# Kernel tuning notes

Hardware: AMD Instinct MI355X
Metric: run time of the kernel (lower is better)

The kernel has to match this reference:

```python
import jax, jax.numpy as jnp
import numpy as np

HEADS = 4
HID = 256
MAX_OFFSET = 2


def setup_inputs() -> dict:
    key = jax.random.key(0)
    ks = jax.random.split(key, 8)
    B, T, C = 4, 512, HID
    x = jax.random.normal(ks[0], (B, T, C), jnp.float32)
    mask = jax.random.randint(ks[1], (B, 1, T), 0, 2).astype(bool)
    s2 = 1.0 / np.sqrt(2 * C)
    s1 = 1.0 / np.sqrt(C)
    W_subj = jax.random.uniform(ks[2], (2 * C, C), jnp.float32, -s2, s2)
    b_subj = jax.random.uniform(ks[3], (C,), jnp.float32, -s2, s2)
    W_obj = jax.random.uniform(ks[4], (2 * C, C), jnp.float32, -s2, s2)
    b_obj = jax.random.uniform(ks[5], (C,), jnp.float32, -s2, s2)
    W_t = jax.random.uniform(ks[6], (C, HEADS), jnp.float32, -s1, s1)
    b_t = jax.random.uniform(ks[7], (HEADS,), jnp.float32, -s1, s1)
    return {"x": x, "W_subj": W_subj, "b_subj": b_subj, "W_obj": W_obj,
            "b_obj": b_obj, "W_t": W_t, "b_t": b_t, "mask": mask}


def reference(x, W_subj, b_subj, W_obj, b_obj, W_t, b_t, mask):
    # x: [B,T,C]. torch MaxPool1d on [B,T,C] pools over the LAST dim (C),
    # kernel = 2*MAX_OFFSET+1, stride 1, same padding (pad value -inf).
    k = 2 * MAX_OFFSET + 1
    x_pooled = jax.lax.reduce_window(
        x, -jnp.inf, jax.lax.max,
        window_dimensions=(1, 1, k), window_strides=(1, 1, 1),
        padding=[(0, 0), (0, 0), (MAX_OFFSET, MAX_OFFSET)])
    x_new = jnp.concatenate([x_pooled, x], axis=2)      # [B,T,2C]
    subj = x_new @ W_subj + b_subj                      # [B,T,C]
    obj = x_new @ W_obj + b_obj                         # [B,T,C]
    # subj.unsqueeze(1): varies over axis 2; obj.unsqueeze(2): varies over axis 1
    abs_multi = jnp.abs(subj[:, None, :, :] - obj[:, :, None, :])  # [B,T,T,C]
    rep = abs_multi @ W_t + b_t                         # [B,T,T,H]
    attn = jax.nn.softmax(jax.nn.relu(rep), axis=2)     # softmax over obj axis
    m = mask[:, 0, :]                                   # [B,T]
    mm = m[:, None, :] & m[:, :, None]                  # [B,T,T]
    attn = jnp.where(mm[..., None], 0.0, attn)          # masked_fill -> 0
    return x_new, attn  # attn[..., h] == attn_adj_list[h]
```

## Files before the change

### kernel.cpp

```cpp
#include <hip/hip_runtime.h>
#include <hip/hip_bf16.h>
#include <math.h>

#define NB 4
#define NT 512
#define NC 256
#define NC2 512
#define NH 4

typedef __attribute__((ext_vector_type(8))) short bf16x8;
typedef __attribute__((ext_vector_type(4))) float f32x4;
typedef __attribute__((ext_vector_type(2))) float f32x2;

__device__ inline unsigned short f2bf(float f) {
    unsigned u = __float_as_uint(f);
    unsigned r = (u + 0x7fffu + ((u >> 16) & 1u)) >> 16;
    return (unsigned short)r;
}

__global__ void k_mask(const unsigned char* __restrict__ raw, int* __restrict__ out) {
    __shared__ int s_bytes;
    if (threadIdx.x == 0) s_bytes = 0;
    __syncthreads();
    int flag = 0;
    const unsigned* w = (const unsigned*)raw;
    for (int i = threadIdx.x; i < (NB * NT) / 4; i += blockDim.x)
        if (w[i] > 1u) flag = 1;
    if (flag) atomicOr(&s_bytes, 1);
    __syncthreads();
    const int ib = s_bytes;
    for (int i = threadIdx.x; i < NB * NT; i += blockDim.x) {
        int v = ib ? (int)raw[i] : ((const int*)raw)[i];
        out[i] = v ? 1 : 0;
    }
}

__global__ void k_pool(const float* __restrict__ x, float* __restrict__ xnew,
                       unsigned short* __restrict__ xb) {
    const int row = blockIdx.x;
    const int c = threadIdx.x;
    __shared__ float r[NC];
    r[c] = x[(size_t)row * NC + c];
    __syncthreads();
    float m = r[c];
    if (c >= 1) m = fmaxf(m, r[c - 1]);
    if (c >= 2) m = fmaxf(m, r[c - 2]);
    if (c <= 254) m = fmaxf(m, r[c + 1]);
    if (c <= 253) m = fmaxf(m, r[c + 2]);
    float* o = xnew + (size_t)row * NC2;
    o[c] = m;
    o[NC + c] = r[c];
    unsigned short* ob = xb + (size_t)row * NC2;
    ob[c] = f2bf(m);
    ob[NC + c] = f2bf(r[c]);
}

__global__ void k_wcast(const float* __restrict__ Ws, const float* __restrict__ Wo,
                        unsigned short* __restrict__ wbt) {
    __shared__ float lds[32][33];
    const int kb = blockIdx.x >> 4;
    const int nb = blockIdx.x & 15;
    const int tx = threadIdx.x & 31;
    const int ty8 = threadIdx.x >> 5;
    const int n0 = nb * 32;
    const int k0 = kb * 32;
    const float* src = (n0 < 256) ? Ws : Wo;
    const int ncol = n0 & 255;
#pragma unroll
    for (int rr = 0; rr < 4; ++rr) {
        int kl = ty8 * 4 + rr;
        lds[kl][tx] = src[(size_t)(k0 + kl) * NC + ncol + tx];
    }
    __syncthreads();
#pragma unroll
    for (int rr = 0; rr < 4; ++rr) {
        int nl = ty8 * 4 + rr;
        wbt[(size_t)(n0 + nl) * NC2 + k0 + tx] = f2bf(lds[tx][nl]);
    }
}

#define MFMA_B16(A, B, C) __builtin_amdgcn_mfma_f32_16x16x32_bf16(A, B, C, 0, 0, 0)
__global__ __launch_bounds__(256) void k_gemm(
    const unsigned short* __restrict__ xb, const unsigned short* __restrict__ wbt,
    const float* __restrict__ bs, const float* __restrict__ bo,
    float* __restrict__ subj, float* __restrict__ obj) {
    const int bx = blockIdx.x;
    const int m0 = (bx >> 3) * 64;
    const int n0 = (bx & 7) * 64;
    const int w = threadIdx.x >> 6, lane = threadIdx.x & 63;
    const int wm = m0 + (w >> 1) * 32;
    const int wn = n0 + (w & 1) * 32;
    const int r = lane & 15, kg = lane >> 4;

    const unsigned short* aB0 = xb + (size_t)(wm + r) * NC2 + kg * 8;
    const unsigned short* aB1 = aB0 + 16 * NC2;
    const unsigned short* bB0 = wbt + (size_t)(wn + r) * NC2 + kg * 8;
    const unsigned short* bB1 = bB0 + 16 * NC2;

    f32x4 acc00 = {0.f, 0.f, 0.f, 0.f}, acc01 = {0.f, 0.f, 0.f, 0.f};
    f32x4 acc10 = {0.f, 0.f, 0.f, 0.f}, acc11 = {0.f, 0.f, 0.f, 0.f};

    bf16x8 a0 = *(const bf16x8*)(aB0);
    bf16x8 a1 = *(const bf16x8*)(aB1);
    bf16x8 b0 = *(const bf16x8*)(bB0);
    bf16x8 b1 = *(const bf16x8*)(bB1);

    for (int kk = 0; kk < NC2; kk += 64) {
        bf16x8 a0n = *(const bf16x8*)(aB0 + kk + 32);
        bf16x8 a1n = *(const bf16x8*)(aB1 + kk + 32);
        bf16x8 b0n = *(const bf16x8*)(bB0 + kk + 32);
        bf16x8 b1n = *(const bf16x8*)(bB1 + kk + 32);
        acc00 = MFMA_B16(a0, b0, acc00);
        acc01 = MFMA_B16(a0, b1, acc01);
        acc10 = MFMA_B16(a1, b0, acc10);
        acc11 = MFMA_B16(a1, b1, acc11);
        if (kk + 64 < NC2) {
            a0 = *(const bf16x8*)(aB0 + kk + 64);
            a1 = *(const bf16x8*)(aB1 + kk + 64);
            b0 = *(const bf16x8*)(bB0 + kk + 64);
            b1 = *(const bf16x8*)(bB1 + kk + 64);
        }
        acc00 = MFMA_B16(a0n, b0n, acc00);
        acc01 = MFMA_B16(a0n, b1n, acc01);
        acc10 = MFMA_B16(a1n, b0n, acc10);
        acc11 = MFMA_B16(a1n, b1n, acc11);
    }

#define EPI(ACC, S, T) { \
    const int col = wn + (T) * 16 + r; \
    const int rowb = wm + (S) * 16 + kg * 4; \
    const float bias = (col < NC) ? bs[col] : bo[col - NC]; \
    float* outp = (col < NC) ? (subj + col) : (obj + col - NC); \
    _Pragma("unroll") \
    for (int e = 0; e < 4; ++e) outp[(size_t)(rowb + e) * NC] = ACC[e] + bias; }
    EPI(acc00, 0, 0) EPI(acc01, 0, 1) EPI(acc10, 1, 0) EPI(acc11, 1, 1)
#undef EPI
}

#define OF32(r) ((r) * 36 + (((r) >> 2) << 2))
__global__ __launch_bounds__(256, 3) void k_rep(
    const float* __restrict__ subj, const float* __restrict__ obj,
    const float* __restrict__ Wt, const float* __restrict__ bt,
    float* __restrict__ attn) {
    const int bx = blockIdx.x;
    const int b = bx >> 8;
    const int rem = bx & 255;
    const int it = rem >> 4, jt = rem & 15;
    const int i0 = it * 32, j0 = jt * 32;
    const int bNT = b * NT;

    __shared__ float lds_buf[4736];
    float* sjT = lds_buf;
    float* obT = lds_buf + 2368;

    const int tid = threadIdx.x;
    const int cs = __builtin_amdgcn_readfirstlane(tid >> 6);
    const int lane = tid & 63;
    const int tx4 = (lane & 7) * 4;
    const int ty4 = (lane >> 3) * 4;
    const int csB = cs * 16;

    const int c4a = tid & 15;
    const int jb = tid >> 4;

    const float4* WtV = (const float4*)Wt;

    f32x2 acc[4][2][4];
#pragma unroll
    for (int ii = 0; ii < 4; ++ii)
#pragma unroll
        for (int jp = 0; jp < 2; ++jp)
#pragma unroll
            for (int h = 0; h < 4; ++h) acc[ii][jp][h] = (f32x2){0.f, 0.f};

    float4 vs0, vs1, vo0, vo1;
#define LOADCH(CC) { \
    vs0 = *(const float4*)(subj + ((size_t)(bNT + j0 + jb)) * NC + (CC) + c4a * 4); \
    vs1 = *(const float4*)(subj + ((size_t)(bNT + j0 + jb + 16)) * NC + (CC) + c4a * 4); \
    vo0 = *(const float4*)(obj  + ((size_t)(bNT + i0 + jb)) * NC + (CC) + c4a * 4); \
    vo1 = *(const float4*)(obj  + ((size_t)(bNT + i0 + jb + 16)) * NC + (CC) + c4a * 4); }

    LOADCH(0)

    for (int cc = 0; cc < 4; ++cc) {
        const int cc64 = cc * 64;
        if (cc) __syncthreads();
        {
            const int rb = c4a * 4;
            sjT[OF32(rb + 0) + jb] = vs0.x; sjT[OF32(rb + 1) + jb] = vs0.y;
            sjT[OF32(rb + 2) + jb] = vs0.z; sjT[OF32(rb + 3) + jb] = vs0.w;
            sjT[OF32(rb + 0) + jb + 16] = vs1.x; sjT[OF32(rb + 1) + jb + 16] = vs1.y;
            sjT[OF32(rb + 2) + jb + 16] = vs1.z; sjT[OF32(rb + 3) + jb + 16] = vs1.w;
            obT[OF32(rb + 0) + jb] = vo0.x; obT[OF32(rb + 1) + jb] = vo0.y;
            obT[OF32(rb + 2) + jb] = vo0.z; obT[OF32(rb + 3) + jb] = vo0.w;
            obT[OF32(rb + 0) + jb + 16] = vo1.x; obT[OF32(rb + 1) + jb + 16] = vo1.y;
            obT[OF32(rb + 2) + jb + 16] = vo1.z; obT[OF32(rb + 3) + jb + 16] = vo1.w;
        }
        __syncthreads();
        if (cc + 1 < 4) LOADCH(cc64 + 64)

#pragma unroll 8
        for (int q = 0; q < 16; ++q) {
            const int cl = csB + q;
            const float4 sv4 = *(const float4*)&sjT[OF32(cl) + tx4];
            const float4 ov4 = *(const float4*)&obT[OF32(cl) + ty4];
            const float4 w4 = WtV[cc64 + cl];
            const f32x2 s01 = {sv4.x, sv4.y};
            const f32x2 s23 = {sv4.z, sv4.w};
            const f32x2 w0 = {w4.x, w4.x};
            const f32x2 w1 = {w4.y, w4.y};
            const f32x2 w2 = {w4.z, w4.z};
            const f32x2 w3 = {w4.w, w4.w};
#define IIBLK(II, OV) { \
    const f32x2 ob2 = {OV, OV}; \
    const f32x2 d01 = s01 - ob2; \
    const f32x2 d23 = s23 - ob2; \
    f32x2 a01, a23; \
    a01.x = fabsf(d01.x); a01.y = fabsf(d01.y); \
    a23.x = fabsf(d23.x); a23.y = fabsf(d23.y); \
    acc[II][0][0] = a01 * w0 + acc[II][0][0]; \
    acc[II][0][1] = a01 * w1 + acc[II][0][1]; \
    acc[II][0][2] = a01 * w2 + acc[II][0][2]; \
    acc[II][0][3] = a01 * w3 + acc[II][0][3]; \
    acc[II][1][0] = a23 * w0 + acc[II][1][0]; \
    acc[II][1][1] = a23 * w1 + acc[II][1][1]; \
    acc[II][1][2] = a23 * w2 + acc[II][1][2]; \
    acc[II][1][3] = a23 * w3 + acc[II][1][3]; }
            IIBLK(0, ov4.x) IIBLK(1, ov4.y) IIBLK(2, ov4.z) IIBLK(3, ov4.w)
#undef IIBLK
        }
    }
#undef LOADCH

    float* rbuf = lds_buf;
    const int lb = lane * 36;
#pragma unroll
    for (int half = 0; half < 2; ++half) {
        __syncthreads();
        if (cs == 1 || cs == 3) {
            float* p = rbuf + ((cs == 1) ? 0 : 2368) + lb;
#pragma unroll
            for (int k = 0; k < 16; ++k)
                *(f32x2*)(p + k * 2) = acc[half * 2 + (k >> 3)][(k >> 2) & 1][k & 3];
        }
        __syncthreads();
        if (cs == 0 || cs == 2) {
            const float* p = rbuf + ((cs == 0) ? 0 : 2368) + lb;
#pragma unroll
            for (int k = 0; k < 16; ++k)
                acc[half * 2 + (k >> 3)][(k >> 2) & 1][k & 3] += *(const f32x2*)(p + k * 2);
        }
    }
#pragma unroll
    for (int half = 0; half < 2; ++half) {
        __syncthreads();
        if (cs == 2) {
            float* p = rbuf + lb;
#pragma unroll
            for (int k = 0; k < 16; ++k)
                *(f32x2*)(p + k * 2) = acc[half * 2 + (k >> 3)][(k >> 2) & 1][k & 3];
        }
        __syncthreads();
        if (cs == 0) {
            const float* p = rbuf + lb;
#pragma unroll
            for (int k = 0; k < 16; ++k)
                acc[half * 2 + (k >> 3)][(k >> 2) & 1][k & 3] += *(const f32x2*)(p + k * 2);
        }
    }

    if (cs == 0) {
        const float4 btv = *(const float4*)bt;
#pragma unroll
        for (int ii = 0; ii < 4; ++ii) {
            const int i = i0 + ty4 + ii;
            float* orow = attn + (((size_t)(bNT + i)) * NT + (j0 + tx4)) * NH;
            float4 r0, r1, r2, r3;
            r0.x = fmaxf(acc[ii][0][0].x + btv.x, 0.f);
            r0.y = fmaxf(acc[ii][0][1].x + btv.y, 0.f);
            r0.z = fmaxf(acc[ii][0][2].x + btv.z, 0.f);
            r0.w = fmaxf(acc[ii][0][3].x + btv.w, 0.f);
            r1.x = fmaxf(acc[ii][0][0].y + btv.x, 0.f);
            r1.y = fmaxf(acc[ii][0][1].y + btv.y, 0.f);
            r1.z = fmaxf(acc[ii][0][2].y + btv.z, 0.f);
            r1.w = fmaxf(acc[ii][0][3].y + btv.w, 0.f);
            r2.x = fmaxf(acc[ii][1][0].x + btv.x, 0.f);
            r2.y = fmaxf(acc[ii][1][1].x + btv.y, 0.f);
            r2.z = fmaxf(acc[ii][1][2].x + btv.z, 0.f);
            r2.w = fmaxf(acc[ii][1][3].x + btv.w, 0.f);
            r3.x = fmaxf(acc[ii][1][0].y + btv.x, 0.f);
            r3.y = fmaxf(acc[ii][1][1].y + btv.y, 0.f);
            r3.z = fmaxf(acc[ii][1][2].y + btv.z, 0.f);
            r3.w = fmaxf(acc[ii][1][3].y + btv.w, 0.f);
            *(float4*)(orow + 0)  = r0;
            *(float4*)(orow + 4)  = r1;
            *(float4*)(orow + 8)  = r2;
            *(float4*)(orow + 12) = r3;
        }
    }
}

__global__ __launch_bounds__(256) void k_soft(float* __restrict__ attn,
                                              const int* __restrict__ mask) {
    const int wv = threadIdx.x >> 6, lane = threadIdx.x & 63;
    const int bi = blockIdx.x * 4 + wv;
    const int b = bi >> 9;
    float4* row = (float4*)(attn + (size_t)bi * (NT * NH));

    float4 v[8];
#pragma unroll
    for (int q = 0; q < 8; ++q) v[q] = row[lane + 64 * q];

    float mx[4];
#pragma unroll
    for (int h = 0; h < 4; ++h) {
        float m = ((const float*)&v[0])[h];
#pragma unroll
        for (int q = 1; q < 8; ++q) m = fmaxf(m, ((const float*)&v[q])[h]);
        mx[h] = m;
    }
#pragma unroll
    for (int off = 32; off; off >>= 1) {
#pragma unroll
        for (int h = 0; h < 4; ++h) mx[h] = fmaxf(mx[h], __shfl_xor(mx[h], off));
    }

    float sm[4] = {0.f, 0.f, 0.f, 0.f};
#pragma unroll
    for (int q = 0; q < 8; ++q) {
        float4 e;
        e.x = expf(v[q].x - mx[0]); e.y = expf(v[q].y - mx[1]);
        e.z = expf(v[q].z - mx[2]); e.w = expf(v[q].w - mx[3]);
        v[q] = e;
        sm[0] += e.x; sm[1] += e.y; sm[2] += e.z; sm[3] += e.w;
    }
#pragma unroll
    for (int off = 32; off; off >>= 1) {
#pragma unroll
        for (int h = 0; h < 4; ++h) sm[h] += __shfl_xor(sm[h], off);
    }
    float rinv[4];
#pragma unroll
    for (int h = 0; h < 4; ++h) rinv[h] = 1.0f / sm[h];

    const int mi = mask[bi];
#pragma unroll
    for (int q = 0; q < 8; ++q) {
        const int mj = mask[b * NT + lane + 64 * q];
        const bool z = (mi & mj);
        float4 o;
        o.x = z ? 0.f : v[q].x * rinv[0];
        o.y = z ? 0.f : v[q].y * rinv[1];
        o.z = z ? 0.f : v[q].z * rinv[2];
        o.w = z ? 0.f : v[q].w * rinv[3];
        row[lane + 64 * q] = o;
    }
}

extern "C" void kernel_launch(void* const* d_in, const int* in_sizes, int n_in,
                              void* d_out, int out_size, void* d_ws, size_t ws_size,
                              hipStream_t stream) {
    const float* x      = (const float*)d_in[0];
    const float* W_subj = (const float*)d_in[1];
    const float* b_subj = (const float*)d_in[2];
    const float* W_obj  = (const float*)d_in[3];
    const float* b_obj  = (const float*)d_in[4];
    const float* W_t    = (const float*)d_in[5];
    const float* b_t    = (const float*)d_in[6];
    const unsigned char* mask_raw = (const unsigned char*)d_in[7];

    float* xnew = (float*)d_out;
    float* attn = xnew + (size_t)NB * NT * NC2;

    int* wmask          = (int*)d_ws;
    float* subj         = (float*)((char*)d_ws + 8192);
    float* obj          = subj + (size_t)NB * NT * NC;
    unsigned short* xb  = (unsigned short*)(obj + (size_t)NB * NT * NC);
    unsigned short* wbt = xb + (size_t)NB * NT * NC2;

    hipLaunchKernelGGL(k_mask, dim3(1), dim3(256), 0, stream, mask_raw, wmask);
    hipLaunchKernelGGL(k_pool, dim3(NB * NT), dim3(NC), 0, stream, x, xnew, xb);
    hipLaunchKernelGGL(k_wcast, dim3(256), dim3(256), 0, stream, W_subj, W_obj, wbt);
    hipLaunchKernelGGL(k_gemm, dim3(256), dim3(256), 0, stream,
                       xb, wbt, b_subj, b_obj, subj, obj);
    hipLaunchKernelGGL(k_rep, dim3(NB * 16 * 16), dim3(256), 0, stream,
                       subj, obj, W_t, b_t, attn);
    hipLaunchKernelGGL(k_soft, dim3(NB * NT / 4), dim3(256), 0, stream, attn, wmask);
}
```

Measured before the change: 137.2 us.

## Rewrite |s-o| as 2*max(s,o)-s-o and fuse prep kernels

The inner rep loop now uses |s-o| = 2*max(s,o) - s - o. This replaces sub+abs with a single max per element, while the linear s·Wt and o·Wt terms are precomputed per row by a new small k_sw kernel and added in the epilogue. The mask, pool and weight-cast kernels are merged into one prep launch to cut launch overhead. The trade-off is one extra kernel launch and slightly different rounding, since the result is now formed as a difference of larger values.

```diff
diff --git a/kernel.cpp b/kernel.cpp
--- a/kernel.cpp
+++ b/kernel.cpp
@@ -18,28 +18,17 @@
     return (unsigned short)r;
 }
 
-__global__ void k_mask(const unsigned char* __restrict__ raw, int* __restrict__ out) {
-    __shared__ int s_bytes;
-    if (threadIdx.x == 0) s_bytes = 0;
-    __syncthreads();
-    int flag = 0;
-    const unsigned* w = (const unsigned*)raw;
-    for (int i = threadIdx.x; i < (NB * NT) / 4; i += blockDim.x)
-        if (w[i] > 1u) flag = 1;
-    if (flag) atomicOr(&s_bytes, 1);
-    __syncthreads();
-    const int ib = s_bytes;
-    for (int i = threadIdx.x; i < NB * NT; i += blockDim.x) {
-        int v = ib ? (int)raw[i] : ((const int*)raw)[i];
-        out[i] = v ? 1 : 0;
-    }
-}
-
-__global__ void k_pool(const float* __restrict__ x, float* __restrict__ xnew,
-                       unsigned short* __restrict__ xb) {
+__global__ __launch_bounds__(256) void k_prep(
+    const float* __restrict__ x, const unsigned char* __restrict__ raw,
+    const float* __restrict__ Ws, const float* __restrict__ Wo,
+    float* __restrict__ xnew, unsigned short* __restrict__ xb,
+    int* __restrict__ wmask, unsigned short* __restrict__ wbt) {
     const int row = blockIdx.x;
     const int c = threadIdx.x;
     __shared__ float r[NC];
+    __shared__ float wl[32][33];
+    __shared__ int s_bytes;
+
     r[c] = x[(size_t)row * NC + c];
     __syncthreads();
     float m = r[c];
@@ -53,29 +42,41 @@
     unsigned short* ob = xb + (size_t)row * NC2;
     ob[c] = f2bf(m);
     ob[NC + c] = f2bf(r[c]);
-}
-
-__global__ void k_wcast(const float* __restrict__ Ws, const float* __restrict__ Wo,
-                        unsigned short* __restrict__ wbt) {
-    __shared__ float lds[32][33];
-    const int kb = blockIdx.x >> 4;
-    const int nb = blockIdx.x & 15;
-    const int tx = threadIdx.x & 31;
-    const int ty8 = threadIdx.x >> 5;
-    const int n0 = nb * 32;
-    const int k0 = kb * 32;
-    const float* src = (n0 < 256) ? Ws : Wo;
-    const int ncol = n0 & 255;
-#pragma unroll
-    for (int rr = 0; rr < 4; ++rr) {
-        int kl = ty8 * 4 + rr;
-        lds[kl][tx] = src[(size_t)(k0 + kl) * NC + ncol + tx];
-    }
-    __syncthreads();
-#pragma unroll
-    for (int rr = 0; rr < 4; ++rr) {
-        int nl = ty8 * 4 + rr;
-        wbt[(size_t)(n0 + nl) * NC2 + k0 + tx] = f2bf(lds[tx][nl]);
+
+    if (row == 0) {
+        if (c == 0) s_bytes = 0;
+        __syncthreads();
+        int flag = 0;
+        const unsigned* w = (const unsigned*)raw;
+        for (int i = c; i < (NB * NT) / 4; i += 256)
+            if (w[i] > 1u) flag = 1;
+        if (flag) atomicOr(&s_bytes, 1);
+        __syncthreads();
+        const int ib = s_bytes;
+        for (int i = c; i < NB * NT; i += 256) {
+            int v = ib ? (int)raw[i] : ((const int*)raw)[i];
+            wmask[i] = v ? 1 : 0;
+        }
+    }
+
+    if (row >= 1 && row <= 256) {
+        const int t = row - 1;
+        const int kb = t >> 4, nb = t & 15;
+        const int tx = c & 31, ty8 = c >> 5;
+        const int n0 = nb * 32, k0 = kb * 32;
+        const float* src = (n0 < 256) ? Ws : Wo;
+        const int ncol = n0 & 255;
+#pragma unroll
+        for (int rr = 0; rr < 4; ++rr) {
+            int kl = ty8 * 4 + rr;
+            wl[kl][tx] = src[(size_t)(k0 + kl) * NC + ncol + tx];
+        }
+        __syncthreads();
+#pragma unroll
+        for (int rr = 0; rr < 4; ++rr) {
+            int nl = ty8 * 4 + rr;
+            wbt[(size_t)(n0 + nl) * NC2 + k0 + tx] = f2bf(wl[tx][nl]);
+        }
     }
 }
 
@@ -137,10 +138,37 @@
 #undef EPI
 }
 
+__global__ __launch_bounds__(256) void k_sw(
+    const float* __restrict__ subj, const float* __restrict__ obj,
+    const float* __restrict__ Wt, float* __restrict__ Sw, float* __restrict__ Ow) {
+    const int gw = blockIdx.x * 4 + (threadIdx.x >> 6);
+    const int lane = threadIdx.x & 63;
+    const int mat = gw & 1;
+    const int row = gw >> 1;
+    const float* src = mat ? obj : subj;
+    const float4 xv = *(const float4*)(src + (size_t)row * NC + lane * 4);
+    const float4* WtV = (const float4*)Wt;
+    float4 a = {0.f, 0.f, 0.f, 0.f};
+#pragma unroll
+    for (int e = 0; e < 4; ++e) {
+        const float4 wv = WtV[lane * 4 + e];
+        const float xe = (e == 0) ? xv.x : (e == 1) ? xv.y : (e == 2) ? xv.z : xv.w;
+        a.x = fmaf(xe, wv.x, a.x); a.y = fmaf(xe, wv.y, a.y);
+        a.z = fmaf(xe, wv.z, a.z); a.w = fmaf(xe, wv.w, a.w);
+    }
+#pragma unroll
+    for (int off = 32; off; off >>= 1) {
+        a.x += __shfl_xor(a.x, off); a.y += __shfl_xor(a.y, off);
+        a.z += __shfl_xor(a.z, off); a.w += __shfl_xor(a.w, off);
+    }
+    if (lane == 0) ((float4*)(mat ? Ow : Sw))[row] = a;
+}
+
 #define OF32(r) ((r) * 36 + (((r) >> 2) << 2))
 __global__ __launch_bounds__(256, 3) void k_rep(
     const float* __restrict__ subj, const float* __restrict__ obj,
     const float* __restrict__ Wt, const float* __restrict__ bt,
+    const float* __restrict__ Sw, const float* __restrict__ Ow,
     float* __restrict__ attn) {
     const int bx = blockIdx.x;
     const int b = bx >> 8;
@@ -213,19 +241,16 @@
             const f32x2 w3 = {w4.w, w4.w};
 #define IIBLK(II, OV) { \
     const f32x2 ob2 = {OV, OV}; \
-    const f32x2 d01 = s01 - ob2; \
-    const f32x2 d23 = s23 - ob2; \
-    f32x2 a01, a23; \
-    a01.x = fabsf(d01.x); a01.y = fabsf(d01.y); \
-    a23.x = fabsf(d23.x); a23.y = fabsf(d23.y); \
-    acc[II][0][0] = a01 * w0 + acc[II][0][0]; \
-    acc[II][0][1] = a01 * w1 + acc[II][0][1]; \
-    acc[II][0][2] = a01 * w2 + acc[II][0][2]; \
-    acc[II][0][3] = a01 * w3 + acc[II][0][3]; \
-    acc[II][1][0] = a23 * w0 + acc[II][1][0]; \
-    acc[II][1][1] = a23 * w1 + acc[II][1][1]; \
-    acc[II][1][2] = a23 * w2 + acc[II][1][2]; \
-    acc[II][1][3] = a23 * w3 + acc[II][1][3]; }
+    const f32x2 m01 = __builtin_elementwise_max(s01, ob2); \
+    const f32x2 m23 = __builtin_elementwise_max(s23, ob2); \
+    acc[II][0][0] = __builtin_elementwise_fma(m01, w0, acc[II][0][0]); \
+    acc[II][0][1] = __builtin_elementwise_fma(m01, w1, acc[II][0][1]); \
+    acc[II][0][2] = __builtin_elementwise_fma(m01, w2, acc[II][0][2]); \
+    acc[II][0][3] = __builtin_elementwise_fma(m01, w3, acc[II][0][3]); \
+    acc[II][1][0] = __builtin_elementwise_fma(m23, w0, acc[II][1][0]); \
+    acc[II][1][1] = __builtin_elementwise_fma(m23, w1, acc[II][1][1]); \
+    acc[II][1][2] = __builtin_elementwise_fma(m23, w2, acc[II][1][2]); \
+    acc[II][1][3] = __builtin_elementwise_fma(m23, w3, acc[II][1][3]); }
             IIBLK(0, ov4.x) IIBLK(1, ov4.y) IIBLK(2, ov4.z) IIBLK(3, ov4.w)
 #undef IIBLK
         }
@@ -271,27 +296,34 @@
 
     if (cs == 0) {
         const float4 btv = *(const float4*)bt;
+        const float4* SwV = (const float4*)Sw;
+        const float4* OwV = (const float4*)Ow;
+        const float4 swv0 = SwV[bNT + j0 + tx4 + 0];
+        const float4 swv1 = SwV[bNT + j0 + tx4 + 1];
+        const float4 swv2 = SwV[bNT + j0 + tx4 + 2];
+        const float4 swv3 = SwV[bNT + j0 + tx4 + 3];
 #pragma unroll
         for (int ii = 0; ii < 4; ++ii) {
             const int i = i0 + ty4 + ii;
+            const float4 owv = OwV[bNT + i];
             float* orow = attn + (((size_t)(bNT + i)) * NT + (j0 + tx4)) * NH;
             float4 r0, r1, r2, r3;
-            r0.x = fmaxf(acc[ii][0][0].x + btv.x, 0.f);
-            r0.y = fmaxf(acc[ii][0][1].x + btv.y, 0.f);
-            r0.z = fmaxf(acc[ii][0][2].x + btv.z, 0.f);
-            r0.w = fmaxf(acc[ii][0][3].x + btv.w, 0.f);
-            r1.x = fmaxf(acc[ii][0][0].y + btv.x, 0.f);
-            r1.y = fmaxf(acc[ii][0][1].y + btv.y, 0.f);
-            r1.z = fmaxf(acc[ii][0][2].y + btv.z, 0.f);
-            r1.w = fmaxf(acc[ii][0][3].y + btv.w, 0.f);
-            r2.x = fmaxf(acc[ii][1][0].x + btv.x, 0.f);
-            r2.y = fmaxf(acc[ii][1][1].x + btv.y, 0.f);
-            r2.z = fmaxf(acc[ii][1][2].x + btv.z, 0.f);
-            r2.w = fmaxf(acc[ii][1][3].x + btv.w, 0.f);
-            r3.x = fmaxf(acc[ii][1][0].y + btv.x, 0.f);
-            r3.y = fmaxf(acc[ii][1][1].y + btv.y, 0.f);
-            r3.z = fmaxf(acc[ii][1][2].y + btv.z, 0.f);
-            r3.w = fmaxf(acc[ii][1][3].y + btv.w, 0.f);
+            r0.x = fmaxf(2.f * acc[ii][0][0].x - swv0.x - owv.x + btv.x, 0.f);
+            r0.y = fmaxf(2.f * acc[ii][0][1].x - swv0.y - owv.y + btv.y, 0.f);
+            r0.z = fmaxf(2.f * acc[ii][0][2].x - swv0.z - owv.z + btv.z, 0.f);
+            r0.w = fmaxf(2.f * acc[ii][0][3].x - swv0.w - owv.w + btv.w, 0.f);
+            r1.x = fmaxf(2.f * acc[ii][0][0].y - swv1.x - owv.x + btv.x, 0.f);
+            r1.y = fmaxf(2.f * acc[ii][0][1].y - swv1.y - owv.y + btv.y, 0.f);
+            r1.z = fmaxf(2.f * acc[ii][0][2].y - swv1.z - owv.z + btv.z, 0.f);
+            r1.w = fmaxf(2.f * acc[ii][0][3].y - swv1.w - owv.w + btv.w, 0.f);
+            r2.x = fmaxf(2.f * acc[ii][1][0].x - swv2.x - owv.x + btv.x, 0.f);
+            r2.y = fmaxf(2.f * acc[ii][1][1].x - swv2.y - owv.y + btv.y, 0.f);
+            r2.z = fmaxf(2.f * acc[ii][1][2].x - swv2.z - owv.z + btv.z, 0.f);
+            r2.w = fmaxf(2.f * acc[ii][1][3].x - swv2.w - owv.w + btv.w, 0.f);
+            r3.x = fmaxf(2.f * acc[ii][1][0].y - swv3.x - owv.x + btv.x, 0.f);
+            r3.y = fmaxf(2.f * acc[ii][1][1].y - swv3.y - owv.y + btv.y, 0.f);
+            r3.z = fmaxf(2.f * acc[ii][1][2].y - swv3.z - owv.z + btv.z, 0.f);
+            r3.w = fmaxf(2.f * acc[ii][1][3].y - swv3.w - owv.w + btv.w, 0.f);
             *(float4*)(orow + 0)  = r0;
             *(float4*)(orow + 4)  = r1;
             *(float4*)(orow + 8)  = r2;
@@ -377,13 +409,16 @@
     float* obj          = subj + (size_t)NB * NT * NC;
     unsigned short* xb  = (unsigned short*)(obj + (size_t)NB * NT * NC);
     unsigned short* wbt = xb + (size_t)NB * NT * NC2;
-
-    hipLaunchKernelGGL(k_mask, dim3(1), dim3(256), 0, stream, mask_raw, wmask);
-    hipLaunchKernelGGL(k_pool, dim3(NB * NT), dim3(NC), 0, stream, x, xnew, xb);
-    hipLaunchKernelGGL(k_wcast, dim3(256), dim3(256), 0, stream, W_subj, W_obj, wbt);
+    float* Sw           = (float*)(wbt + (size_t)NC2 * NC2);
+    float* Ow           = Sw + (size_t)NB * NT * NH;
+
+    hipLaunchKernelGGL(k_prep, dim3(NB * NT), dim3(256), 0, stream,
+                       x, mask_raw, W_subj, W_obj, xnew, xb, wmask, wbt);
     hipLaunchKernelGGL(k_gemm, dim3(256), dim3(256), 0, stream,
                        xb, wbt, b_subj, b_obj, subj, obj);
+    hipLaunchKernelGGL(k_sw, dim3(1024), dim3(256), 0, stream,
+                       subj, obj, W_t, Sw, Ow);
     hipLaunchKernelGGL(k_rep, dim3(NB * 16 * 16), dim3(256), 0, stream,
-                       subj, obj, W_t, b_t, attn);
+                       subj, obj, W_t, b_t, Sw, Ow, attn);
     hipLaunchKernelGGL(k_soft, dim3(NB * NT / 4), dim3(256), 0, stream, attn, wmask);
 }
```

New measurement: 138.1 us. No clear change (+0.6%).
